# Optimization experiments

Measured on AMD Instinct MI355X. Metric: run time of the kernel, lower is better.

The kernel has to match this reference:

```python
import jax, jax.numpy as jnp
import numpy as np

N_NODES = 100000
N_EDGES = 3200000
N_FEAT = 512
HIDDEN = 16
N_CLASSES = 64


def setup_inputs() -> dict:
    key = jax.random.key(0)
    k1, k2, k3, k4 = jax.random.split(key, 4)
    x = jax.random.normal(k1, (N_NODES, N_FEAT), dtype=jnp.float32)
    edge_index = jax.random.randint(k2, (2, N_EDGES), 0, N_NODES, dtype=jnp.int64)
    # Glorot-ish scaling keeps log_softmax numerically tame
    W1 = jax.random.normal(k3, (N_FEAT, HIDDEN), dtype=jnp.float32) / np.sqrt(N_FEAT)
    b1 = jnp.zeros((HIDDEN,), dtype=jnp.float32)
    W2 = jax.random.normal(k4, (HIDDEN, N_CLASSES), dtype=jnp.float32) / np.sqrt(HIDDEN)
    b2 = jnp.zeros((N_CLASSES,), dtype=jnp.float32)
    return {"x": x, "edge_index": edge_index, "W1": W1, "b1": b1, "W2": W2, "b2": b2}


def _gcn_conv(h, src, dst, norm, W, b, num_nodes):
    # dense transform first (PyG GCNConv order), then normalized scatter-add
    h = h @ W                                   # [N, out]
    msg = h[src] * norm[:, None]                # gather + edge scaling [E, out]
    agg = jax.ops.segment_sum(msg, dst, num_segments=num_nodes)
    return agg + b


def reference(x, edge_index, W1, b1, W2, b2):
    N = x.shape[0]
    loop = jnp.arange(N, dtype=edge_index.dtype)
    src = jnp.concatenate([edge_index[0], loop])  # add self-loops
    dst = jnp.concatenate([edge_index[1], loop])
    deg = jax.ops.segment_sum(jnp.ones_like(src, dtype=x.dtype), dst, num_segments=N)
    dinv = jax.lax.rsqrt(jnp.maximum(deg, 1.0))
    norm = dinv[src] * dinv[dst]                  # symmetric D^-1/2 A_hat D^-1/2

    h = jax.nn.relu(_gcn_conv(x, src, dst, norm, W1, b1, N))
    # dropout: identity in eval mode (training=False)
    h = _gcn_conv(h, src, dst, norm, W2, b2, N)
    return jax.nn.log_softmax(h, axis=1)
```

## Files before the change

kernel.cpp:

```cpp
#include <hip/hip_runtime.h>

#define NNODES 100000
#define NEDGES 3200000
#define NFEAT  512
#define NHID   16
#define NCLS   64
#define NB     391
#define CAP    10240
#define EPB    8192

typedef short bf16x8 __attribute__((ext_vector_type(8)));
typedef float f32x4  __attribute__((ext_vector_type(4)));

__device__ __forceinline__ short f2bf(float f) {
    unsigned u = __float_as_uint(f);
    return (short)((u + 0x7FFFu + ((u >> 16) & 1u)) >> 16);
}

__global__ __launch_bounds__(512) void k_part(const int* __restrict__ src,
                                              const int* __restrict__ dst,
                                              unsigned* __restrict__ gcnt,
                                              unsigned* __restrict__ part) {
    __shared__ unsigned hist[NB];
    __shared__ unsigned scn[512];
    __shared__ unsigned cursor[NB];
    __shared__ unsigned delta[NB];
    __shared__ unsigned staged[EPB];
    __shared__ unsigned short pbkt[EPB];
    int t = threadIdx.x;
    int base = blockIdx.x * EPB;
    int nblk = min(EPB, NEDGES - base);
    for (int i = t; i < NB; i += 512) hist[i] = 0;
    __syncthreads();
    unsigned pk[16]; unsigned short bk[16];
#pragma unroll
    for (int j = 0; j < 16; ++j) {
        int o = t + j * 512;
        if (o < nblk) {
            int s = src[base + o], d = dst[base + o];
            pk[j] = (unsigned)s | ((unsigned)(d & 255) << 17);
            bk[j] = (unsigned short)(d >> 8);
            atomicAdd(&hist[bk[j]], 1u);
        } else bk[j] = 0xFFFFu;
    }
    __syncthreads();
    scn[t] = (t < NB) ? hist[t] : 0u;
    __syncthreads();
#pragma unroll
    for (int off = 1; off < 512; off <<= 1) {
        unsigned a = (t >= off) ? scn[t - off] : 0u;
        __syncthreads();
        scn[t] += a;
        __syncthreads();
    }
    for (int i = t; i < NB; i += 512) {
        unsigned h = hist[i];
        unsigned ex = scn[i] - h;
        cursor[i] = ex;
        unsigned gb = h ? atomicAdd(&gcnt[i], h) : 0u;
        delta[i] = (unsigned)i * CAP + gb - ex;
    }
    __syncthreads();
#pragma unroll
    for (int j = 0; j < 16; ++j) {
        if (bk[j] != 0xFFFFu) {
            unsigned p = atomicAdd(&cursor[bk[j]], 1u);
            staged[p] = pk[j];
            pbkt[p] = bk[j];
        }
    }
    __syncthreads();
    for (int i = t; i < nblk; i += 512) {
        unsigned b = pbkt[i];
        unsigned d = delta[b] + (unsigned)i;
        if (d < (b + 1u) * CAP) part[d] = staged[i];
    }
}

__global__ __launch_bounds__(512) void k_csr(const unsigned* __restrict__ gcnt,
                                             unsigned* __restrict__ part,
                                             unsigned* __restrict__ offs,
                                             unsigned* __restrict__ cnt,
                                             float* __restrict__ dinv) {
    __shared__ unsigned hist[256], nst[256], cursor[256];
    __shared__ unsigned staged[CAP];
    int t = threadIdx.x, b = blockIdx.x;
    unsigned cb = min(gcnt[b], (unsigned)CAP);
    unsigned* seg = part + (size_t)b * CAP;
    if (t < 256) hist[t] = 0;
    __syncthreads();
    for (unsigned i = t; i < cb; i += 512)
        atomicAdd(&hist[(seg[i] >> 17) & 255u], 1u);
    __syncthreads();
    if (t < 256) nst[t] = hist[t];
    __syncthreads();
#pragma unroll
    for (int off = 1; off < 256; off <<= 1) {
        unsigned a = (t >= off && t < 256) ? nst[t - off] : 0u;
        __syncthreads();
        if (t < 256) nst[t] += a;
        __syncthreads();
    }
    if (t < 256) {
        unsigned ex = nst[t] - hist[t];
        cursor[t] = ex;
        int node = b * 256 + t;
        if (node < NNODES) {
            offs[node] = (unsigned)b * CAP + ex;
            cnt[node] = hist[t];
            dinv[node] = rsqrtf((float)hist[t] + 1.f);
        }
    }
    __syncthreads();
    for (unsigned i = t; i < cb; i += 512) {
        unsigned p = seg[i];
        unsigned r = atomicAdd(&cursor[(p >> 17) & 255u], 1u);
        staged[r] = p & 0x1FFFFu;
    }
    __syncthreads();
    for (unsigned i = t; i < cb; i += 512)
        seg[i] = staged[i];
}

__global__ __launch_bounds__(256) void k_gemm1(const float* __restrict__ x,
                                               const float* __restrict__ w1,
                                               const float* __restrict__ dinv,
                                               float* __restrict__ hs1) {
    __shared__ short w1t[16][520];
    int tid = threadIdx.x;
    for (int idx = tid; idx < NFEAT * NHID; idx += 256) {
        int k = idx >> 4, n = idx & 15;
        w1t[n][k] = f2bf(w1[idx]);
    }
    __syncthreads();
    int wave = tid >> 6, lane = tid & 63;
    int tile = blockIdx.x * 4 + wave;
    if (tile >= NNODES / 16) return;
    int m = lane & 15, q = lane >> 4;
    const float* xrow = x + (size_t)(tile * 16 + m) * NFEAT + q * 8;
    const short* wrow = &w1t[m][q * 8];
    f32x4 acc = {0.f, 0.f, 0.f, 0.f};
#pragma unroll
    for (int kb = 0; kb < NFEAT / 32; ++kb) {
        float4 a0 = *(const float4*)(xrow + kb * 32);
        float4 a1 = *(const float4*)(xrow + kb * 32 + 4);
        bf16x8 a;
        a[0] = f2bf(a0.x); a[1] = f2bf(a0.y); a[2] = f2bf(a0.z); a[3] = f2bf(a0.w);
        a[4] = f2bf(a1.x); a[5] = f2bf(a1.y); a[6] = f2bf(a1.z); a[7] = f2bf(a1.w);
        bf16x8 b = *(const bf16x8*)(wrow + kb * 32);
        acc = __builtin_amdgcn_mfma_f32_16x16x32_bf16(a, b, acc, 0, 0, 0);
    }
    float* out = hs1 + (size_t)(tile * 16) * NHID;
#pragma unroll
    for (int r = 0; r < 4; ++r) {
        int row = q * 4 + r;
        out[row * NHID + m] = acc[r] * dinv[tile * 16 + row];
    }
}

__global__ __launch_bounds__(256) void k_agg1(const unsigned* __restrict__ offs,
                                              const unsigned* __restrict__ cnt,
                                              const unsigned* __restrict__ eb,
                                              const float* __restrict__ hs1,
                                              const float* __restrict__ dinv,
                                              const float* __restrict__ b1,
                                              float* __restrict__ hs2) {
    int tid = threadIdx.x;
    int node = blockIdx.x * 4 + (tid >> 6);
    int lane = tid & 63, f = lane & 15, slot = lane >> 4;
    unsigned start = offs[node];
    int deg = (int)cnt[node];
    float acc = 0.f;
    int rounds = (deg + 15) >> 4;
    int cl = deg - 1;
    for (int r = 0; r < rounds; ++r) {
        int jb = r * 16 + slot * 4;
        int j0 = min(jb,     cl), j1 = min(jb + 1, cl);
        int j2 = min(jb + 2, cl), j3 = min(jb + 3, cl);
        unsigned e0 = eb[start + j0], e1 = eb[start + j1];
        unsigned e2 = eb[start + j2], e3 = eb[start + j3];
        float a0 = hs1[(size_t)e0 * NHID + f];
        float a1 = hs1[(size_t)e1 * NHID + f];
        float a2 = hs1[(size_t)e2 * NHID + f];
        float a3 = hs1[(size_t)e3 * NHID + f];
        acc += (jb     < deg ? a0 : 0.f);
        acc += (jb + 1 < deg ? a1 : 0.f);
        acc += (jb + 2 < deg ? a2 : 0.f);
        acc += (jb + 3 < deg ? a3 : 0.f);
    }
    acc += __shfl_xor(acc, 16);
    acc += __shfl_xor(acc, 32);
    float di = dinv[node];
    float v = (acc + hs1[(size_t)node * NHID + f]) * di + b1[f];
    v = v > 0.f ? v : 0.f;
    if (slot == 0) hs2[(size_t)node * NHID + f] = v * di;
}

__global__ __launch_bounds__(256) void k_out2(const unsigned* __restrict__ offs,
                                              const unsigned* __restrict__ cnt,
                                              const unsigned* __restrict__ eb,
                                              const float* __restrict__ hs2,
                                              const float* __restrict__ dinv,
                                              const float* __restrict__ w2,
                                              const float* __restrict__ b2,
                                              float* __restrict__ out) {
    __shared__ float w2f[NHID * NCLS];
    __shared__ float b2f[NCLS];
    int tid = threadIdx.x;
    for (int i = tid; i < NHID * NCLS; i += 256) w2f[i] = w2[i];
    if (tid < NCLS) b2f[tid] = b2[tid];
    __syncthreads();
    int node = blockIdx.x * 4 + (tid >> 6);
    int lane = tid & 63, f = lane & 15, slot = lane >> 4;
    unsigned start = offs[node];
    int deg = (int)cnt[node];
    float acc = 0.f;
    int rounds = (deg + 15) >> 4;
    int cl = deg - 1;
    for (int r = 0; r < rounds; ++r) {
        int jb = r * 16 + slot * 4;
        int j0 = min(jb,     cl), j1 = min(jb + 1, cl);
        int j2 = min(jb + 2, cl), j3 = min(jb + 3, cl);
        unsigned e0 = eb[start + j0], e1 = eb[start + j1];
        unsigned e2 = eb[start + j2], e3 = eb[start + j3];
        float a0 = hs2[(size_t)e0 * NHID + f];
        float a1 = hs2[(size_t)e1 * NHID + f];
        float a2 = hs2[(size_t)e2 * NHID + f];
        float a3 = hs2[(size_t)e3 * NHID + f];
        acc += (jb     < deg ? a0 : 0.f);
        acc += (jb + 1 < deg ? a1 : 0.f);
        acc += (jb + 2 < deg ? a2 : 0.f);
        acc += (jb + 3 < deg ? a3 : 0.f);
    }
    acc += __shfl_xor(acc, 16);
    acc += __shfl_xor(acc, 32);
    float di = dinv[node];
    float v = (acc + hs2[(size_t)node * NHID + f]) * di;
    float logit = b2f[lane];
#pragma unroll
    for (int k = 0; k < NHID; ++k)
        logit += __shfl(v, k) * w2f[k * NCLS + lane];
    float mx = logit;
#pragma unroll
    for (int off = 32; off > 0; off >>= 1) mx = fmaxf(mx, __shfl_xor(mx, off));
    float ex = __expf(logit - mx);
    float s = ex;
#pragma unroll
    for (int off = 32; off > 0; off >>= 1) s += __shfl_xor(s, off);
    out[(size_t)node * NCLS + lane] = logit - mx - logf(s);
}

extern "C" void kernel_launch(void* const* d_in, const int* in_sizes, int n_in,
                              void* d_out, int out_size, void* d_ws, size_t ws_size,
                              hipStream_t stream) {
    const float* x  = (const float*)d_in[0];
    const int*   ei = (const int*)d_in[1];
    const float* w1 = (const float*)d_in[2];
    const float* b1 = (const float*)d_in[3];
    const float* w2 = (const float*)d_in[4];
    const float* b2 = (const float*)d_in[5];
    const int* src = ei;
    const int* dst = ei + NEDGES;

    char* ws = (char*)d_ws;
    unsigned* gcnt = (unsigned*)(ws + 0);
    unsigned* offs = (unsigned*)(ws + 2048);
    unsigned* cnt  = (unsigned*)(ws + 402048);
    float*    dinv = (float*)   (ws + 802048);
    float*    hs1  = (float*)   (ws + 1202048);
    float*    hs2  = (float*)   (ws + 7602048);
    unsigned* part = (unsigned*)(ws + 14002048);

    hipMemsetAsync(gcnt, 0, 2048, stream);
    k_part <<<NB, 512, 0, stream>>>(src, dst, gcnt, part);
    k_csr  <<<NB, 512, 0, stream>>>(gcnt, part, offs, cnt, dinv);
    k_gemm1<<<(NNODES / 16 + 3) / 4, 256, 0, stream>>>(x, w1, dinv, hs1);
    k_agg1 <<<NNODES / 4, 256, 0, stream>>>(offs, cnt, part, hs1, dinv, b1, hs2);
    k_out2 <<<NNODES / 4, 256, 0, stream>>>(offs, cnt, part, hs2, dinv, w2, b2, (float*)d_out);
}
```

Measured before the change: 466.8 us.

## Store hidden features as bf16 and widen gather unroll in aggregation kernels

```diff
diff --git a/kernel.cpp b/kernel.cpp
--- a/kernel.cpp
+++ b/kernel.cpp
@@ -15,6 +15,9 @@
 __device__ __forceinline__ short f2bf(float f) {
     unsigned u = __float_as_uint(f);
     return (short)((u + 0x7FFFu + ((u >> 16) & 1u)) >> 16);
+}
+__device__ __forceinline__ float bf2f(unsigned short u) {
+    return __uint_as_float((unsigned)u << 16);
 }
 
 __global__ __launch_bounds__(512) void k_part(const int* __restrict__ src,
@@ -125,7 +128,7 @@
 __global__ __launch_bounds__(256) void k_gemm1(const float* __restrict__ x,
                                                const float* __restrict__ w1,
                                                const float* __restrict__ dinv,
-                                               float* __restrict__ hs1) {
+                                               unsigned short* __restrict__ hs1) {
     __shared__ short w1t[16][520];
     int tid = threadIdx.x;
     for (int idx = tid; idx < NFEAT * NHID; idx += 256) {
@@ -150,96 +153,87 @@
         bf16x8 b = *(const bf16x8*)(wrow + kb * 32);
         acc = __builtin_amdgcn_mfma_f32_16x16x32_bf16(a, b, acc, 0, 0, 0);
     }
-    float* out = hs1 + (size_t)(tile * 16) * NHID;
+    unsigned short* out = hs1 + (size_t)(tile * 16) * NHID;
 #pragma unroll
     for (int r = 0; r < 4; ++r) {
         int row = q * 4 + r;
-        out[row * NHID + m] = acc[r] * dinv[tile * 16 + row];
+        out[row * NHID + m] = (unsigned short)f2bf(acc[r] * dinv[tile * 16 + row]);
     }
 }
 
 __global__ __launch_bounds__(256) void k_agg1(const unsigned* __restrict__ offs,
                                               const unsigned* __restrict__ cnt,
                                               const unsigned* __restrict__ eb,
-                                              const float* __restrict__ hs1,
+                                              const unsigned short* __restrict__ hs1,
                                               const float* __restrict__ dinv,
                                               const float* __restrict__ b1,
-                                              float* __restrict__ hs2) {
+                                              unsigned short* __restrict__ hs2) {
     int tid = threadIdx.x;
     int node = blockIdx.x * 4 + (tid >> 6);
     int lane = tid & 63, f = lane & 15, slot = lane >> 4;
     unsigned start = offs[node];
     int deg = (int)cnt[node];
+    float di = dinv[node];
     float acc = 0.f;
-    int rounds = (deg + 15) >> 4;
+    int rounds = (deg + 31) >> 5;
     int cl = deg - 1;
     for (int r = 0; r < rounds; ++r) {
-        int jb = r * 16 + slot * 4;
-        int j0 = min(jb,     cl), j1 = min(jb + 1, cl);
-        int j2 = min(jb + 2, cl), j3 = min(jb + 3, cl);
-        unsigned e0 = eb[start + j0], e1 = eb[start + j1];
-        unsigned e2 = eb[start + j2], e3 = eb[start + j3];
-        float a0 = hs1[(size_t)e0 * NHID + f];
-        float a1 = hs1[(size_t)e1 * NHID + f];
-        float a2 = hs1[(size_t)e2 * NHID + f];
-        float a3 = hs1[(size_t)e3 * NHID + f];
-        acc += (jb     < deg ? a0 : 0.f);
-        acc += (jb + 1 < deg ? a1 : 0.f);
-        acc += (jb + 2 < deg ? a2 : 0.f);
-        acc += (jb + 3 < deg ? a3 : 0.f);
+        int jb = r * 32 + slot * 8;
+        unsigned e[8];
+#pragma unroll
+        for (int u = 0; u < 8; ++u) e[u] = eb[start + min(jb + u, cl)];
+        float a[8];
+#pragma unroll
+        for (int u = 0; u < 8; ++u) a[u] = bf2f(hs1[(size_t)e[u] * NHID + f]);
+#pragma unroll
+        for (int u = 0; u < 8; ++u) acc += (jb + u < deg) ? a[u] : 0.f;
     }
     acc += __shfl_xor(acc, 16);
     acc += __shfl_xor(acc, 32);
-    float di = dinv[node];
-    float v = (acc + hs1[(size_t)node * NHID + f]) * di + b1[f];
+    float v = (acc + bf2f(hs1[(size_t)node * NHID + f])) * di + b1[f];
     v = v > 0.f ? v : 0.f;
-    if (slot == 0) hs2[(size_t)node * NHID + f] = v * di;
+    if (slot == 0) hs2[(size_t)node * NHID + f] = (unsigned short)f2bf(v * di);
 }
 
 __global__ __launch_bounds__(256) void k_out2(const unsigned* __restrict__ offs,
                                               const unsigned* __restrict__ cnt,
                                               const unsigned* __restrict__ eb,
-                                              const float* __restrict__ hs2,
+                                              const unsigned short* __restrict__ hs2,
                                               const float* __restrict__ dinv,
                                               const float* __restrict__ w2,
                                               const float* __restrict__ b2,
                                               float* __restrict__ out) {
-    __shared__ float w2f[NHID * NCLS];
-    __shared__ float b2f[NCLS];
     int tid = threadIdx.x;
-    for (int i = tid; i < NHID * NCLS; i += 256) w2f[i] = w2[i];
-    if (tid < NCLS) b2f[tid] = b2[tid];
-    __syncthreads();
     int node = blockIdx.x * 4 + (tid >> 6);
     int lane = tid & 63, f = lane & 15, slot = lane >> 4;
     unsigned start = offs[node];
     int deg = (int)cnt[node];
+    float di = dinv[node];
+    float w2c[NHID];
+#pragma unroll
+    for (int k = 0; k < NHID; ++k) w2c[k] = w2[k * NCLS + lane];
+    float bb = b2[lane];
     float acc = 0.f;
-    int rounds = (deg + 15) >> 4;
+    int rounds = (deg + 31) >> 5;
     int cl = deg - 1;
     for (int r = 0; r < rounds; ++r) {
-        int jb = r * 16 + slot * 4;
-        int j0 = min(jb,     cl), j1 = min(jb + 1, cl);
-        int j2 = min(jb + 2, cl), j3 = min(jb + 3, cl);
-        unsigned e0 = eb[start + j0], e1 = eb[start + j1];
-        unsigned e2 = eb[start + j2], e3 = eb[start + j3];
-        float a0 = hs2[(size_t)e0 * NHID + f];
-        float a1 = hs2[(size_t)e1 * NHID + f];
-        float a2 = hs2[(size_t)e2 * NHID + f];
-        float a3 = hs2[(size_t)e3 * NHID + f];
-        acc += (jb     < deg ? a0 : 0.f);
-        acc += (jb + 1 < deg ? a1 : 0.f);
-        acc += (jb + 2 < deg ? a2 : 0.f);
-        acc += (jb + 3 < deg ? a3 : 0.f);
+        int jb = r * 32 + slot * 8;
+        unsigned e[8];
+#pragma unroll
+        for (int u = 0; u < 8; ++u) e[u] = eb[start + min(jb + u, cl)];
+        float a[8];
+#pragma unroll
+        for (int u = 0; u < 8; ++u) a[u] = bf2f(hs2[(size_t)e[u] * NHID + f]);
+#pragma unroll
+        for (int u = 0; u < 8; ++u) acc += (jb + u < deg) ? a[u] : 0.f;
     }
     acc += __shfl_xor(acc, 16);
     acc += __shfl_xor(acc, 32);
-    float di = dinv[node];
-    float v = (acc + hs2[(size_t)node * NHID + f]) * di;
-    float logit = b2f[lane];
+    float v = (acc + bf2f(hs2[(size_t)node * NHID + f])) * di;
+    float logit = bb;
 #pragma unroll
     for (int k = 0; k < NHID; ++k)
-        logit += __shfl(v, k) * w2f[k * NCLS + lane];
+        logit += __shfl(v, k) * w2c[k];
     float mx = logit;
 #pragma unroll
     for (int off = 32; off > 0; off >>= 1) mx = fmaxf(mx, __shfl_xor(mx, off));
@@ -267,9 +261,9 @@
     unsigned* offs = (unsigned*)(ws + 2048);
     unsigned* cnt  = (unsigned*)(ws + 402048);
     float*    dinv = (float*)   (ws + 802048);
-    float*    hs1  = (float*)   (ws + 1202048);
-    float*    hs2  = (float*)   (ws + 7602048);
-    unsigned* part = (unsigned*)(ws + 14002048);
+    unsigned short* hs1 = (unsigned short*)(ws + 1202048);
+    unsigned short* hs2 = (unsigned short*)(ws + 4402048);
+    unsigned* part = (unsigned*)(ws + 7602048);
 
     hipMemsetAsync(gcnt, 0, 2048, stream);
     k_part <<<NB, 512, 0, stream>>>(src, dst, gcnt, part);
```

Result: faster. 437.6 us (-6.3%).
